# Optimization experiments

Measured on AMD Instinct MI355X. Metric: run time of the kernel, lower is better.

The kernel has to match this reference:

```python
import math
import jax, jax.numpy as jnp
import numpy as np

B, S, DIM = 1, 2048, 2880
N_HEADS, N_KV, HD = 64, 8, 64
ROPE_FACTOR = 32.0
THETA = 150000.0
NEG_INF = -1e30


def setup_inputs() -> dict:
    key = jax.random.key(0)
    ks = jax.random.split(key, 12)
    std = 0.02
    x = jax.random.normal(ks[0], (B, S, DIM), jnp.float32)
    # rope cache: (S, 2*HD) = [cos | sin], rotate_half convention (angles duplicated)
    inv_freq = 1.0 / (THETA ** (np.arange(0, HD, 2, dtype=np.float32) / HD))
    angles = np.arange(S, dtype=np.float32)[:, None] * inv_freq[None, :]   # (S, HD/2)
    emb = np.concatenate([angles, angles], axis=-1)                        # (S, HD)
    rope_cache = jnp.asarray(np.concatenate([np.cos(emb), np.sin(emb)], axis=-1))  # (S, 2*HD)
    wq_w = jax.random.normal(ks[1], (N_HEADS * HD, DIM), jnp.float32) * std
    wq_b = jax.random.normal(ks[2], (N_HEADS * HD,), jnp.float32) * std
    wk_w = jax.random.normal(ks[3], (N_KV * HD, DIM), jnp.float32) * std
    wk_b = jax.random.normal(ks[4], (N_KV * HD,), jnp.float32) * std
    wv_w = jax.random.normal(ks[5], (N_KV * HD, DIM), jnp.float32) * std
    wv_b = jax.random.normal(ks[6], (N_KV * HD,), jnp.float32) * std
    wo_w = jax.random.normal(ks[7], (DIM, N_HEADS * HD), jnp.float32) * std
    wo_b = jax.random.normal(ks[8], (DIM,), jnp.float32) * std
    sinks = jax.random.normal(ks[9], (N_HEADS,), jnp.float32) * std
    return {"x": x, "rope_cache": rope_cache, "wq_w": wq_w, "wq_b": wq_b,
            "wk_w": wk_w, "wk_b": wk_b, "wv_w": wv_w, "wv_b": wv_b,
            "wo_w": wo_w, "wo_b": wo_b, "sinks": sinks, "sliding_window": 128}


def _rotate_half(t):
    t1, t2 = t[..., : HD // 2], t[..., HD // 2 :]
    return jnp.concatenate([-t2, t1], axis=-1)


def reference(x, rope_cache, wq_w, wq_b, wk_w, wk_b, wv_w, wv_b, wo_w, wo_b, sinks, sliding_window):
    bsz, seqlen, _ = x.shape
    mscale = 0.1 * math.log(ROPE_FACTOR) + 1.0
    scale = mscale / math.sqrt(HD)

    q = (x @ wq_w.T + wq_b).reshape(bsz, seqlen, N_HEADS, HD)
    k = (x @ wk_w.T + wk_b).reshape(bsz, seqlen, N_KV, HD)
    v = (x @ wv_w.T + wv_b).reshape(bsz, seqlen, N_KV, HD)

    cos = rope_cache[:seqlen, :HD][None, :, None, :]   # (1,S,1,HD)
    sin = rope_cache[:seqlen, HD:][None, :, None, :]
    q = q * cos + _rotate_half(q) * sin
    k = k * cos + _rotate_half(k) * sin

    q = q.transpose(0, 2, 1, 3)                        # (B,H,S,hd)
    n_rep = N_HEADS // N_KV
    k = jnp.repeat(k.transpose(0, 2, 1, 3), n_rep, axis=1)  # GQA expand
    v = jnp.repeat(v.transpose(0, 2, 1, 3), n_rep, axis=1)

    scores = jnp.einsum("bhqd,bhkd->bhqk", q, k) * scale
    i = jnp.arange(seqlen)[:, None]
    j = jnp.arange(seqlen)[None, :]
    mask = (j <= i) & ((i - j) < sliding_window)       # causal + sliding window
    scores = jnp.where(mask[None, None], scores, NEG_INF)

    lse = jax.nn.logsumexp(scores, axis=-1)            # (B,H,S)
    attn = jax.nn.softmax(scores, axis=-1)
    out = jnp.einsum("bhqk,bhkd->bhqd", attn, v)

    sink_scale = jax.nn.sigmoid(lse - sinks[None, :, None])[..., None]
    out = out * sink_scale

    out = out.transpose(0, 2, 1, 3).reshape(bsz, seqlen, N_HEADS * HD)
    return out @ wo_w.T + wo_b
```

## Files before the change

### kernel.cpp

```cpp
#include <hip/hip_runtime.h>
#include <hip/hip_bf16.h>
#include <math.h>
#include <stdint.h>


typedef __bf16 bf16x8 __attribute__((ext_vector_type(8)));
typedef float  f32x4  __attribute__((ext_vector_type(4)));
typedef uint32_t u32x4 __attribute__((ext_vector_type(4)));

#define MFMA_BF16(a,b,c) __builtin_amdgcn_mfma_f32_16x16x32_bf16((a),(b),(c),0,0,0)

#define XB   0L
#define WQB  5898240L
#define WKB  17694720L
#define WVB  19169280L
#define WOB  20643840L
#define QB   32440320L
#define KB   40828928L
#define VB   41877504L

__device__ __forceinline__ void gld_lds16(const void* g, void* l) {
    __builtin_amdgcn_global_load_lds(
        (__attribute__((address_space(1))) void*)(g),
        (__attribute__((address_space(3))) void*)(l), 16, 0, 0);
}

__device__ __forceinline__ bf16x8 ld8f(const float* p) {
    f32x4 a = *(const f32x4*)p;
    f32x4 b = *(const f32x4*)(p + 4);
    bf16x8 r;
#pragma unroll
    for (int t = 0; t < 4; t++) { r[t] = (__bf16)a[t]; r[t + 4] = (__bf16)b[t]; }
    return r;
}

__device__ __forceinline__ uint32_t pack2(float a, float b) {
    __bf16 x = (__bf16)a, y = (__bf16)b;
    return (uint32_t)__builtin_bit_cast(unsigned short, x)
         | ((uint32_t)__builtin_bit_cast(unsigned short, y) << 16);
}

__global__ __launch_bounds__(256) void convert_kernel(
    const float* __restrict__ x,  const float* __restrict__ wq,
    const float* __restrict__ wk, const float* __restrict__ wv,
    const float* __restrict__ wo, __bf16* __restrict__ dst)
{
    long e = ((long)blockIdx.x * 256 + threadIdx.x) * 8;
    const float* src; long off;
    if      (e <  WQB) { src = x;  off = e; }
    else if (e <  WKB) { src = wq; off = e - WQB; }
    else if (e <  WVB) { src = wk; off = e - WKB; }
    else if (e <  WOB) { src = wv; off = e - WVB; }
    else               { src = wo; off = e - WOB; }
    *(bf16x8*)(dst + e) = ld8f(src + off);
}

__device__ __forceinline__ void stage_half(
    const __bf16* p0, const __bf16* p1, int kk, __bf16* dst, int tid)
{
    gld_lds16(p0 + kk, dst + tid * 8);
    gld_lds16(p1 + kk, dst + 4096 + tid * 8);
}

__device__ __forceinline__ void gemm256(
    const __bf16* __restrict__ A, const __bf16* __restrict__ W,
    const float* __restrict__ bias, __bf16* __restrict__ C,
    int N, int Ks, int kBeg, int kEnd, int m0, int n0,
    __bf16* As, __bf16* Bs)
{
    const int tid  = threadIdx.x;
    const int lane = tid & 63;
    const int wv   = tid >> 6;
    const int wr   = wv >> 2;
    const int wc   = wv & 3;
    const int quad = lane >> 4;
    const int c    = lane & 15;
    const int fxor = c & 7;
    const int lrB  = (wc & 1) * 64;

    const int srow = tid >> 3;
    const int scg  = (tid & 7) ^ (srow & 7);

    const __bf16* pa[4]; const __bf16* pb[4];
#pragma unroll
    for (int g = 0; g < 4; g++) {
        pa[g] = A + (size_t)(m0 + g * 64 + srow) * Ks + scg * 8;
        int br = n0 + g * 64 + srow; if (br > N - 1) br = N - 1;
        pb[g] = W + (size_t)br * Ks + scg * 8;
    }

    const int NT = (kEnd - kBeg) >> 6;

    f32x4 acc[8][4];
#pragma unroll
    for (int i = 0; i < 8; i++)
#pragma unroll
        for (int j = 0; j < 4; j++) acc[i][j] = (f32x4){0.f, 0.f, 0.f, 0.f};

    stage_half(pb[0], pb[1], kBeg, Bs,        tid);
    stage_half(pa[0], pa[1], kBeg, As,        tid);
    stage_half(pa[2], pa[3], kBeg, As + 8192, tid);
    stage_half(pb[2], pb[3], kBeg, Bs + 8192, tid);
    if (NT > 1) {
        stage_half(pb[0], pb[1], kBeg + 64, Bs + 16384, tid);
        stage_half(pa[0], pa[1], kBeg + 64, As + 16384, tid);
        asm volatile("s_waitcnt vmcnt(4)" ::: "memory");
    } else {
        asm volatile("s_waitcnt vmcnt(0)" ::: "memory");
    }
    __builtin_amdgcn_sched_barrier(0);
    __builtin_amdgcn_s_barrier();

    bf16x8 af[4][2], bb[4][2];

    for (int t = 0; t < NT; ++t) {
        const int d = t & 1;
        const __bf16* Ab = As + d * 16384 + wr * 8192;
        const __bf16* Bb = Bs + d * 16384 + (wc >> 1) * 8192;
        __bf16* Asn = As + (d ^ 1) * 16384;
        __bf16* Bsn = Bs + (d ^ 1) * 16384;
        __bf16* Asc = As + d * 16384;
        __bf16* Bsc = Bs + d * 16384;
        const int kk1 = kBeg + (t + 1) * 64;
        const int kk2 = kBeg + (t + 2) * 64;

        __builtin_amdgcn_sched_barrier(0);
#pragma unroll
        for (int m = 0; m < 4; m++)
#pragma unroll
            for (int kt = 0; kt < 2; kt++)
                af[m][kt] = *(const bf16x8*)&Ab[(m * 16 + c) * 64 + (((kt * 4 + quad) ^ fxor) * 8)];
#pragma unroll
        for (int j = 0; j < 2; j++)
#pragma unroll
            for (int kt = 0; kt < 2; kt++)
                bb[j][kt] = *(const bf16x8*)&Bb[(lrB + j * 16 + c) * 64 + (((kt * 4 + quad) ^ fxor) * 8)];
        if (t + 1 < NT) stage_half(pa[2], pa[3], kk1, Asn + 8192, tid);
        __builtin_amdgcn_sched_barrier(0);
        __builtin_amdgcn_s_barrier();
        asm volatile("s_waitcnt lgkmcnt(0)" ::: "memory");
        __builtin_amdgcn_sched_barrier(0);
        __builtin_amdgcn_s_setprio(1);
#pragma unroll
        for (int i = 0; i < 4; i++)
#pragma unroll
            for (int j = 0; j < 2; j++)
#pragma unroll
                for (int kt = 0; kt < 2; kt++)
                    acc[i][j] = MFMA_BF16(af[i][kt], bb[j][kt], acc[i][j]);
        __builtin_amdgcn_s_setprio(0);
        __builtin_amdgcn_sched_barrier(0);
        __builtin_amdgcn_s_barrier();

        __builtin_amdgcn_sched_barrier(0);
#pragma unroll
        for (int j = 2; j < 4; j++)
#pragma unroll
            for (int kt = 0; kt < 2; kt++)
                bb[j][kt] = *(const bf16x8*)&Bb[(lrB + j * 16 + c) * 64 + (((kt * 4 + quad) ^ fxor) * 8)];
        if (t + 1 < NT) stage_half(pb[2], pb[3], kk1, Bsn + 8192, tid);
        __builtin_amdgcn_sched_barrier(0);
        __builtin_amdgcn_s_barrier();
        asm volatile("s_waitcnt lgkmcnt(0)" ::: "memory");
        __builtin_amdgcn_sched_barrier(0);
        __builtin_amdgcn_s_setprio(1);
#pragma unroll
        for (int i = 0; i < 4; i++)
#pragma unroll
            for (int j = 2; j < 4; j++)
#pragma unroll
                for (int kt = 0; kt < 2; kt++)
                    acc[i][j] = MFMA_BF16(af[i][kt], bb[j][kt], acc[i][j]);
        __builtin_amdgcn_s_setprio(0);
        __builtin_amdgcn_sched_barrier(0);
        __builtin_amdgcn_s_barrier();

        __builtin_amdgcn_sched_barrier(0);
#pragma unroll
        for (int m = 0; m < 4; m++)
#pragma unroll
            for (int kt = 0; kt < 2; kt++)
                af[m][kt] = *(const bf16x8*)&Ab[((m + 4) * 16 + c) * 64 + (((kt * 4 + quad) ^ fxor) * 8)];
        if (t + 2 < NT) stage_half(pb[0], pb[1], kk2, Bsc, tid);
        __builtin_amdgcn_sched_barrier(0);
        __builtin_amdgcn_s_barrier();
        asm volatile("s_waitcnt lgkmcnt(0)" ::: "memory");
        __builtin_amdgcn_sched_barrier(0);
        __builtin_amdgcn_s_setprio(1);
#pragma unroll
        for (int i = 0; i < 4; i++)
#pragma unroll
            for (int j = 0; j < 2; j++)
#pragma unroll
                for (int kt = 0; kt < 2; kt++)
                    acc[i + 4][j] = MFMA_BF16(af[i][kt], bb[j][kt], acc[i + 4][j]);
        __builtin_amdgcn_s_setprio(0);
        __builtin_amdgcn_sched_barrier(0);
        __builtin_amdgcn_s_barrier();

        __builtin_amdgcn_sched_barrier(0);
        if (t + 2 < NT) {
            stage_half(pa[0], pa[1], kk2, Asc, tid);
            asm volatile("s_waitcnt vmcnt(4)" ::: "memory");
        } else if (t + 1 < NT) {
            asm volatile("s_waitcnt vmcnt(0)" ::: "memory");
        }
        __builtin_amdgcn_sched_barrier(0);
        __builtin_amdgcn_s_barrier();
        __builtin_amdgcn_sched_barrier(0);
        __builtin_amdgcn_s_setprio(1);
#pragma unroll
        for (int i = 0; i < 4; i++)
#pragma unroll
            for (int j = 2; j < 4; j++)
#pragma unroll
                for (int kt = 0; kt < 2; kt++)
                    acc[i + 4][j] = MFMA_BF16(af[i][kt], bb[j][kt], acc[i + 4][j]);
        __builtin_amdgcn_s_setprio(0);
        __builtin_amdgcn_sched_barrier(0);
        __builtin_amdgcn_s_barrier();
    }

#pragma unroll
    for (int j = 0; j < 4; j++) {
        int col = n0 + wc * 64 + j * 16 + c;
        if (col >= N) continue;
        float bv = bias ? bias[col] : 0.0f;
#pragma unroll
        for (int i = 0; i < 8; i++) {
            int row = m0 + wr * 128 + i * 16 + quad * 4;
#pragma unroll
            for (int r = 0; r < 4; r++)
                C[(size_t)(row + r) * N + col] = (__bf16)(acc[i][j][r] + bv);
        }
    }
}

__global__ __launch_bounds__(512, 2) void qkv_kernel(
    const __bf16* __restrict__ x,
    const __bf16* __restrict__ wq, const float* __restrict__ bq,
    const __bf16* __restrict__ wk, const float* __restrict__ bk,
    const __bf16* __restrict__ wv, const float* __restrict__ bv,
    __bf16* __restrict__ qo, __bf16* __restrict__ ko, __bf16* __restrict__ vo)
{
    __shared__ __align__(16) __bf16 As[2 * 16384], Bs[2 * 16384];
    const int lin = blockIdx.y * 8 + blockIdx.x;
    const int wg  = (lin & 7) * 20 + (lin >> 3);
    const int m0  = (wg & 7) * 256;
    const int by2 = wg >> 3;
    const __bf16 *W; const float* bias; __bf16* C; int N, n0;
    if (by2 < 16)      { W = wq; bias = bq; C = qo; N = 4096; n0 = by2 * 256; }
    else if (by2 < 18) { W = wk; bias = bk; C = ko; N = 512;  n0 = (by2 - 16) * 256; }
    else               { W = wv; bias = bv; C = vo; N = 512;  n0 = (by2 - 18) * 256; }
    gemm256(x, W, bias, C, N, 2880, 0, 2880, m0, n0, As, Bs);
}

__global__ __launch_bounds__(512, 2) void oproj_kernel(
    const __bf16* __restrict__ a, const __bf16* __restrict__ w,
    __bf16* __restrict__ p0, __bf16* __restrict__ p1)
{
    __shared__ __align__(16) __bf16 As[2 * 16384], Bs[2 * 16384];
    const int z = blockIdx.z;
    __bf16* C = z ? p1 : p0;
    const int lin = blockIdx.y * 8 + blockIdx.x;
    const int wg  = (lin & 7) * 12 + (lin >> 3);
    const int m0  = (wg & 7) * 256;
    const int by2 = wg >> 3;
    gemm256(a, w, nullptr, C, 2880, 4096, z * 2048, (z + 1) * 2048,
            m0, by2 * 256, As, Bs);
}

__global__ __launch_bounds__(256) void reduce_kernel(
    const __bf16* __restrict__ p0, const __bf16* __restrict__ p1,
    const float* __restrict__ bo, float* __restrict__ out)
{
    long e = ((long)blockIdx.x * 256 + threadIdx.x) * 8;
    int col = (int)(e % 2880L);
    bf16x8 a = *(const bf16x8*)(p0 + e);
    bf16x8 b = *(const bf16x8*)(p1 + e);
    f32x4 o0, o1;
#pragma unroll
    for (int t = 0; t < 4; t++) {
        o0[t] = (float)a[t]     + (float)b[t]     + bo[col + t];
        o1[t] = (float)a[4 + t] + (float)b[4 + t] + bo[col + 4 + t];
    }
    *(f32x4*)(out + e)     = o0;
    *(f32x4*)(out + e + 4) = o1;
}

template<int F>
__device__ __forceinline__ void attn_f_step(
    const __bf16* __restrict__ Ks, const __bf16* __restrict__ Vt,
    __bf16* __restrict__ q, bf16x8 qf0, bf16x8 qf1,
    int i0, int h, int k0, float sk,
    int c, int quad, int laneA, int laneB, bool hiSel, int db)
{
    f32x4 acc9[9];
#pragma unroll
    for (int jj = 0; jj < 9; jj++) acc9[jj] = (f32x4){0.f, 0.f, 0.f, 0.f};
    __builtin_amdgcn_s_setprio(1);
#pragma unroll
    for (int jj = 0; jj < 9; jj++) {
        const int j = F + jj;
        bf16x8 kf0 = *(const bf16x8*)&Ks[(j * 16 + c) * 72 + quad * 8];
        bf16x8 kf1 = *(const bf16x8*)&Ks[(j * 16 + c) * 72 + 32 + quad * 8];
        acc9[jj] = MFMA_BF16(kf0, qf0, acc9[jj]);
        acc9[jj] = MFMA_BF16(kf1, qf1, acc9[jj]);
    }
    __builtin_amdgcn_s_setprio(0);

    const int jgb = k0 + F * 16 + quad * 4;
    float rmax = -3.0e4f;
#pragma unroll
    for (int jj = 0; jj < 9; jj++)
#pragma unroll
        for (int r = 0; r < 4; r++) {
            int d  = db  - jj * 16 - r;
            int jg = jgb + jj * 16 + r;
            bool ok = ((unsigned)d < 128u) && (jg >= 0);
            float vv = ok ? acc9[jj][r] : -3.0e4f;
            acc9[jj][r] = vv;
            rmax = fmaxf(rmax, vv);
        }
    rmax = fmaxf(rmax, __shfl_xor(rmax, 16));
    rmax = fmaxf(rmax, __shfl_xor(rmax, 32));

    float rs = 0.f;
#pragma unroll
    for (int jj = 0; jj < 9; jj++)
#pragma unroll
        for (int r = 0; r < 4; r++) {
            float e = __expf(acc9[jj][r] - rmax);
            acc9[jj][r] = e;
            rs += e;
        }
    rs += __shfl_xor(rs, 16);
    rs += __shfl_xor(rs, 32);

    float s   = fmaxf(rs, 1e-20f);
    float lse = rmax + __logf(s);
    float fac = 1.f / ((1.f + __expf(sk - lse)) * s);

    uint32_t pk[20];
#pragma unroll
    for (int t = 0; t < 20; t++) pk[t] = 0;
#pragma unroll
    for (int jj = 0; jj < 9; jj++) {
        const int li = (F & 1) ? (2 * jj + 2) : (2 * jj);
        pk[li]     = pack2(acc9[jj][0] * fac, acc9[jj][1] * fac);
        pk[li + 1] = pack2(acc9[jj][2] * fac, acc9[jj][3] * fac);
    }

    f32x4 acc2[4];
#pragma unroll
    for (int jd = 0; jd < 4; jd++) acc2[jd] = (f32x4){0.f, 0.f, 0.f, 0.f};
#pragma unroll
    for (int kk = 0; kk < 5; kk++) {
        const int kt = (F >> 1) + kk;
        uint32_t l0  = (uint32_t)__shfl((int)pk[4 * kk],     laneA);
        uint32_t h0  = (uint32_t)__shfl((int)pk[4 * kk + 1], laneA);
        uint32_t l0b = (uint32_t)__shfl((int)pk[4 * kk],     laneB);
        uint32_t h0b = (uint32_t)__shfl((int)pk[4 * kk + 1], laneB);
        uint32_t l1  = (uint32_t)__shfl((int)pk[4 * kk + 2], laneA);
        uint32_t h1  = (uint32_t)__shfl((int)pk[4 * kk + 3], laneA);
        uint32_t l1b = (uint32_t)__shfl((int)pk[4 * kk + 2], laneB);
        uint32_t h1b = (uint32_t)__shfl((int)pk[4 * kk + 3], laneB);
        u32x4 wvv = { hiSel ? l1  : l0,  hiSel ? h1  : h0,
                      hiSel ? l1b : l0b, hiSel ? h1b : h0b };
        bf16x8 pa = __builtin_bit_cast(bf16x8, wvv);
        __builtin_amdgcn_s_setprio(1);
#pragma unroll
        for (int jd = 0; jd < 4; jd++) {
            bf16x8 bv = *(const bf16x8*)&Vt[(jd * 16 + c) * 200 + kt * 32 + quad * 8];
            acc2[jd] = MFMA_BF16(pa, bv, acc2[jd]);
        }
        __builtin_amdgcn_s_setprio(0);
    }

#pragma unroll
    for (int jd = 0; jd < 4; jd++)
#pragma unroll
        for (int r = 0; r < 4; r++)
            q[(size_t)(i0 + F * 16 + quad * 4 + r) * 4096 + h * 64 + jd * 16 + c]
                = (__bf16)acc2[jd][r];
}

__global__ __launch_bounds__(512) void attn_kernel(
    __bf16* __restrict__ q, const __bf16* __restrict__ k,
    const __bf16* __restrict__ v, const float* __restrict__ sinks,
    const float* __restrict__ rope)
{
    __shared__ __align__(16) __bf16 Ks[192 * 72];
    __shared__ __align__(16) __bf16 Vt[64 * 200];

    const int tid = threadIdx.x, lane = tid & 63, w = tid >> 6;
    const int quad = lane >> 4, c = lane & 15;
    const int i0  = blockIdx.x * 64;
    const int kvh = blockIdx.y;
    const int h   = kvh * 8 + w;
    const int k0  = i0 - 128;
    const float scale = 0.16832169878499658f;

#pragma unroll
    for (int it = 0; it < 2; it++) {
        int unit = it * 512 + tid;
        if (unit < 768) {
            int krow = unit >> 2;
            int kdg  = (unit & 3) * 8;
            int j = k0 + krow; if (j < 0) j = 0;
            const __bf16* gp = k + (size_t)j * 512 + kvh * 64 + kdg;
            bf16x8 x1 = *(const bf16x8*)(gp);
            bf16x8 x2 = *(const bf16x8*)(gp + 32);
            const float* rc = rope + (size_t)j * 128 + kdg;
            bf16x8 o1, o2;
#pragma unroll
            for (int t = 0; t < 8; t++) {
                float cc = rc[t], si = rc[64 + t];
                float a = (float)x1[t], b = (float)x2[t];
                o1[t] = (__bf16)(a * cc - b * si);
                o2[t] = (__bf16)(b * cc + a * si);
            }
            *(bf16x8*)&Ks[krow * 72 + kdg]      = o1;
            *(bf16x8*)&Ks[krow * 72 + kdg + 32] = o2;
        }
    }

    {
        const int vrow = tid & 63;
        const int d0   = (tid >> 6) * 8;
#pragma unroll
        for (int it = 0; it < 3; it++) {
            int s = it * 64 + vrow;
            int j = k0 + s; if (j < 0) j = 0;
            bf16x8 t = *(const bf16x8*)(v + (size_t)j * 512 + kvh * 64 + d0);
#pragma unroll
            for (int u = 0; u < 8; u++) Vt[(d0 + u) * 200 + s] = t[u];
        }
    }

    bf16x8 qf[4][2];
#pragma unroll
    for (int f = 0; f < 4; f++) {
        const int row = i0 + f * 16 + c;
        const __bf16* gp = q + (size_t)row * 4096 + h * 64 + quad * 8;
        bf16x8 x1 = *(const bf16x8*)(gp);
        bf16x8 x2 = *(const bf16x8*)(gp + 32);
        const float* rc = rope + (size_t)row * 128 + quad * 8;
        bf16x8 o1, o2;
#pragma unroll
        for (int t = 0; t < 8; t++) {
            float cc = rc[t] * scale, si = rc[64 + t] * scale;
            float a = (float)x1[t], b = (float)x2[t];
            o1[t] = (__bf16)(a * cc - b * si);
            o2[t] = (__bf16)(b * cc + a * si);
        }
        qf[f][0] = o1; qf[f][1] = o2;
    }

    __syncthreads();

    const float sk   = sinks[h];
    const int laneA  = ((quad & 1) << 5) + c;
    const int laneB  = laneA + 16;
    const bool hiSel = (quad >> 1) != 0;
    const int db     = 128 + c - quad * 4;

    attn_f_step<0>(Ks, Vt, q, qf[0][0], qf[0][1], i0, h, k0, sk, c, quad, laneA, laneB, hiSel, db);
    attn_f_step<1>(Ks, Vt, q, qf[1][0], qf[1][1], i0, h, k0, sk, c, quad, laneA, laneB, hiSel, db);
    attn_f_step<2>(Ks, Vt, q, qf[2][0], qf[2][1], i0, h, k0, sk, c, quad, laneA, laneB, hiSel, db);
    attn_f_step<3>(Ks, Vt, q, qf[3][0], qf[3][1], i0, h, k0, sk, c, quad, laneA, laneB, hiSel, db);
}

extern "C" void kernel_launch(void* const* d_in, const int* in_sizes, int n_in,
                              void* d_out, int out_size, void* d_ws, size_t ws_size,
                              hipStream_t stream) {
    const float* x    = (const float*)d_in[0];
    const float* rope = (const float*)d_in[1];
    const float* wq   = (const float*)d_in[2];
    const float* bq   = (const float*)d_in[3];
    const float* wk   = (const float*)d_in[4];
    const float* bk   = (const float*)d_in[5];
    const float* wv   = (const float*)d_in[6];
    const float* bv   = (const float*)d_in[7];
    const float* wo   = (const float*)d_in[8];
    const float* bo   = (const float*)d_in[9];
    const float* sk   = (const float*)d_in[10];
    float* out = (float*)d_out;

    __bf16* wsb = (__bf16*)d_ws;
    __bf16* xb  = wsb + XB;
    __bf16* wqb = wsb + WQB;
    __bf16* wkb = wsb + WKB;
    __bf16* wvb = wsb + WVB;
    __bf16* wob = wsb + WOB;
    __bf16* qb  = wsb + QB;
    __bf16* kb  = wsb + KB;
    __bf16* vb  = wsb + VB;
    __bf16* po0 = wsb + 0L;
    __bf16* po1 = wsb + 5898240L;

    convert_kernel<<<15840, 256, 0, stream>>>(x, wq, wk, wv, wo, xb);
    qkv_kernel<<<dim3(8, 20), 512, 0, stream>>>(xb, wqb, bq, wkb, bk, wvb, bv,
                                                qb, kb, vb);
    attn_kernel<<<dim3(32, 8), 512, 0, stream>>>(qb, kb, vb, sk, rope);
    oproj_kernel<<<dim3(8, 12, 2), 512, 0, stream>>>(qb, wob, po0, po1);
    reduce_kernel<<<2880, 256, 0, stream>>>(po0, po1, bo, out);
}
```

Baseline: 361.3 us.

## Use 128x128 tile GEMM for output projection and reorder MFMA loops

Replaces the 256x256 pipelined GEMM in the output projection with a simpler 128x128-tile, 256-thread kernel launched on a 16x23x2 grid with an XCD-aware remap. This raises the workgroup count from 192 to 736 to fill more CUs. The trade-off is lower data reuse per tile and a non-pipelined, unswizzled LDS load loop with full syncthreads barriers. Separately, the MFMA loops in the shared 256 GEMM are reordered to put kt outermost, which changes the dependency spacing between accumulator updates.

After: 354.3 us. No clear change (-1.9%).

```diff
diff --git a/kernel.cpp b/kernel.cpp
--- a/kernel.cpp
+++ b/kernel.cpp
@@ -53,6 +53,78 @@
     else if (e <  WOB) { src = wv; off = e - WVB; }
     else               { src = wo; off = e - WOB; }
     *(bf16x8*)(dst + e) = ld8f(src + off);
+}
+
+__device__ __forceinline__ void gemm_block64(
+    const __bf16* __restrict__ A, const __bf16* __restrict__ W,
+    const float* __restrict__ bias, __bf16* __restrict__ C,
+    int N, int Ks, int kBeg, int kEnd, int m0, int n0,
+    __bf16* As, __bf16* Bs)
+{
+    const int tid  = threadIdx.x;
+    const int lane = tid & 63;
+    const int wv   = tid >> 6;
+    const int wm   = (wv >> 1) * 64;
+    const int wn   = (wv & 1) * 64;
+    const int quad = lane >> 4;
+    const int c    = lane & 15;
+
+    const int srow = tid >> 2;
+    const int scol = (tid & 3) * 8;
+
+    int br0 = n0 + srow;      if (br0 > N - 1) br0 = N - 1;
+    int br1 = n0 + 64 + srow; if (br1 > N - 1) br1 = N - 1;
+    const __bf16* pa0 = A + (size_t)(m0 + srow) * Ks + scol;
+    const __bf16* pa1 = A + (size_t)(m0 + 64 + srow) * Ks + scol;
+    const __bf16* pb0 = W + (size_t)br0 * Ks + scol;
+    const __bf16* pb1 = W + (size_t)br1 * Ks + scol;
+
+    f32x4 acc[4][4];
+#pragma unroll
+    for (int i = 0; i < 4; i++)
+#pragma unroll
+        for (int j = 0; j < 4; j++) acc[i][j] = (f32x4){0.f, 0.f, 0.f, 0.f};
+
+    for (int kk = kBeg; kk < kEnd; kk += 64) {
+        gld_lds16(pa0 + kk,      As + tid * 8);
+        gld_lds16(pa1 + kk,      As + 2048 + tid * 8);
+        gld_lds16(pa0 + kk + 32, As + 4096 + tid * 8);
+        gld_lds16(pa1 + kk + 32, As + 6144 + tid * 8);
+        gld_lds16(pb0 + kk,      Bs + tid * 8);
+        gld_lds16(pb1 + kk,      Bs + 2048 + tid * 8);
+        gld_lds16(pb0 + kk + 32, Bs + 4096 + tid * 8);
+        gld_lds16(pb1 + kk + 32, Bs + 6144 + tid * 8);
+        __syncthreads();
+        for (int kt = 0; kt < 2; kt++) {
+            bf16x8 af[4], bfv[4];
+#pragma unroll
+            for (int i = 0; i < 4; i++)
+                af[i] = *(const bf16x8*)&As[kt * 4096 + (wm + i * 16 + c) * 32 + quad * 8];
+#pragma unroll
+            for (int j = 0; j < 4; j++)
+                bfv[j] = *(const bf16x8*)&Bs[kt * 4096 + (wn + j * 16 + c) * 32 + quad * 8];
+#pragma unroll
+            for (int i = 0; i < 4; i++)
+#pragma unroll
+                for (int j = 0; j < 4; j++)
+                    acc[i][j] = MFMA_BF16(af[i], bfv[j], acc[i][j]);
+        }
+        __syncthreads();
+    }
+
+#pragma unroll
+    for (int j = 0; j < 4; j++) {
+        int col = n0 + wn + j * 16 + c;
+        if (col >= N) continue;
+        float bv = bias ? bias[col] : 0.0f;
+#pragma unroll
+        for (int i = 0; i < 4; i++) {
+            int row = m0 + wm + i * 16 + quad * 4;
+#pragma unroll
+            for (int r = 0; r < 4; r++)
+                C[(size_t)(row + r) * N + col] = (__bf16)(acc[i][j][r] + bv);
+        }
+    }
 }
 
 __device__ __forceinline__ void stage_half(
@@ -142,11 +214,11 @@
         __builtin_amdgcn_sched_barrier(0);
         __builtin_amdgcn_s_setprio(1);
 #pragma unroll
-        for (int i = 0; i < 4; i++)
-#pragma unroll
-            for (int j = 0; j < 2; j++)
-#pragma unroll
-                for (int kt = 0; kt < 2; kt++)
+        for (int kt = 0; kt < 2; kt++)
+#pragma unroll
+            for (int i = 0; i < 4; i++)
+#pragma unroll
+                for (int j = 0; j < 2; j++)
                     acc[i][j] = MFMA_BF16(af[i][kt], bb[j][kt], acc[i][j]);
         __builtin_amdgcn_s_setprio(0);
         __builtin_amdgcn_sched_barrier(0);
@@ -165,11 +237,11 @@
         __builtin_amdgcn_sched_barrier(0);
         __builtin_amdgcn_s_setprio(1);
 #pragma unroll
-        for (int i = 0; i < 4; i++)
-#pragma unroll
-            for (int j = 2; j < 4; j++)
-#pragma unroll
-                for (int kt = 0; kt < 2; kt++)
+        for (int kt = 0; kt < 2; kt++)
+#pragma unroll
+            for (int i = 0; i < 4; i++)
+#pragma unroll
+                for (int j = 2; j < 4; j++)
                     acc[i][j] = MFMA_BF16(af[i][kt], bb[j][kt], acc[i][j]);
         __builtin_amdgcn_s_setprio(0);
         __builtin_amdgcn_sched_barrier(0);
@@ -188,11 +260,11 @@
         __builtin_amdgcn_sched_barrier(0);
         __builtin_amdgcn_s_setprio(1);
 #pragma unroll
-        for (int i = 0; i < 4; i++)
-#pragma unroll
-            for (int j = 0; j < 2; j++)
-#pragma unroll
-                for (int kt = 0; kt < 2; kt++)
+        for (int kt = 0; kt < 2; kt++)
+#pragma unroll
+            for (int i = 0; i < 4; i++)
+#pragma unroll
+                for (int j = 0; j < 2; j++)
                     acc[i + 4][j] = MFMA_BF16(af[i][kt], bb[j][kt], acc[i + 4][j]);
         __builtin_amdgcn_s_setprio(0);
         __builtin_amdgcn_sched_barrier(0);
@@ -210,11 +282,11 @@
         __builtin_amdgcn_sched_barrier(0);
         __builtin_amdgcn_s_setprio(1);
 #pragma unroll
-        for (int i = 0; i < 4; i++)
-#pragma unroll
-            for (int j = 2; j < 4; j++)
-#pragma unroll
-                for (int kt = 0; kt < 2; kt++)
+        for (int kt = 0; kt < 2; kt++)
+#pragma unroll
+            for (int i = 0; i < 4; i++)
+#pragma unroll
+                for (int j = 2; j < 4; j++)
                     acc[i + 4][j] = MFMA_BF16(af[i][kt], bb[j][kt], acc[i + 4][j]);
         __builtin_amdgcn_s_setprio(0);
         __builtin_amdgcn_sched_barrier(0);
@@ -255,19 +327,19 @@
     gemm256(x, W, bias, C, N, 2880, 0, 2880, m0, n0, As, Bs);
 }
 
-__global__ __launch_bounds__(512, 2) void oproj_kernel(
+__global__ __launch_bounds__(256, 3) void oproj_kernel(
     const __bf16* __restrict__ a, const __bf16* __restrict__ w,
     __bf16* __restrict__ p0, __bf16* __restrict__ p1)
 {
-    __shared__ __align__(16) __bf16 As[2 * 16384], Bs[2 * 16384];
+    __shared__ __align__(16) __bf16 As[8192], Bs[8192];
     const int z = blockIdx.z;
     __bf16* C = z ? p1 : p0;
-    const int lin = blockIdx.y * 8 + blockIdx.x;
-    const int wg  = (lin & 7) * 12 + (lin >> 3);
-    const int m0  = (wg & 7) * 256;
-    const int by2 = wg >> 3;
-    gemm256(a, w, nullptr, C, 2880, 4096, z * 2048, (z + 1) * 2048,
-            m0, by2 * 256, As, Bs);
+    const int orig = blockIdx.y * 16 + blockIdx.x;
+    const int wg   = (orig & 7) * 46 + (orig >> 3);
+    const int bx   = wg & 15;
+    const int by   = wg >> 4;
+    gemm_block64(a, w, nullptr, C, 2880, 4096, z * 2048, (z + 1) * 2048,
+                 bx * 128, by * 128, As, Bs);
 }
 
 __global__ __launch_bounds__(256) void reduce_kernel(
@@ -503,6 +575,6 @@
     qkv_kernel<<<dim3(8, 20), 512, 0, stream>>>(xb, wqb, bq, wkb, bk, wvb, bv,
                                                 qb, kb, vb);
     attn_kernel<<<dim3(32, 8), 512, 0, stream>>>(qb, kb, vb, sk, rope);
-    oproj_kernel<<<dim3(8, 12, 2), 512, 0, stream>>>(qb, wob, po0, po1);
+    oproj_kernel<<<dim3(16, 23, 2), 256, 0, stream>>>(qb, wob, po0, po1);
     reduce_kernel<<<2880, 256, 0, stream>>>(po0, po1, bo, out);
 }
```
